# Optimization experiments

Measured on AMD Instinct MI355X. Metric: run time of the kernel, lower is better.

## Reference

```python
import jax, jax.numpy as jnp
import numpy as np

N_NODES = 100000
N_EDGES = 1600000
N_GRAPHS = 64
EMB_DIM = 64
DIMS = [6, 16, 32, 64, EMB_DIM]


def setup_inputs() -> dict:
    key = jax.random.key(0)
    ks = jax.random.split(key, 16)
    feat = jax.random.normal(ks[0], (N_NODES, DIMS[0]), dtype=jnp.float32)
    src = jax.random.randint(ks[1], (N_EDGES,), 0, N_NODES)
    dst = jax.random.randint(ks[2], (N_EDGES,), 0, N_NODES)
    graph_ids = jnp.sort(jax.random.randint(ks[3], (N_NODES,), 0, N_GRAPHS))
    inp = {"feat": feat, "src": src, "dst": dst, "graph_ids": graph_ids}
    # fc_neigh weights for each SAGEConv (gcn aggregator has no fc_self), Xavier-ish init
    for i in range(4):
        din, dout = DIMS[i], DIMS[i + 1]
        scale = 1.0 / np.sqrt(din)
        inp[f"W{i+1}"] = jax.random.uniform(ks[4 + 2 * i], (din, dout), jnp.float32, -scale, scale)
        inp[f"b{i+1}"] = jnp.zeros((dout,), jnp.float32)
    return inp


def _sage_gcn(feat, src, dst, deg, W, b):
    # DGL SAGEConv aggregator_type='gcn':
    # h_neigh = (sum_{u in N(v)} h_u + h_v) / (in_deg(v) + 1); out = h_neigh @ W + b
    neigh = jax.ops.segment_sum(feat[src], dst, num_segments=N_NODES)  # [N, din]
    h = (neigh + feat) / (deg[:, None] + 1.0)
    return h @ W + b


def reference(feat, src, dst, graph_ids, W1, b1, W2, b2, W3, b3, W4, b4):
    deg = jax.ops.segment_sum(jnp.ones((N_EDGES,), feat.dtype), dst, num_segments=N_NODES)
    h = feat
    for W, b in ((W1, b1), (W2, b2), (W3, b3), (W4, b4)):
        h = jax.nn.relu(_sage_gcn(h, src, dst, deg, W, b))
    # dgl.mean_nodes: per-graph mean over nodes
    sums = jax.ops.segment_sum(h, graph_ids, num_segments=N_GRAPHS)          # [G, emb]
    cnts = jax.ops.segment_sum(jnp.ones((N_NODES,), h.dtype), graph_ids, num_segments=N_GRAPHS)
    return sums / jnp.maximum(cnts, 1.0)[:, None]
```

## Files before the change

### kernel.cpp

```cpp
#include <hip/hip_runtime.h>
#include <hip/hip_bf16.h>
#include <hip/hip_fp16.h>

#define N_NODES 100000
#define N_EDGES 1600000
#define N_GRAPHS 64

#define NB_BKT 256
#define NPBKT 391
#define EPB 4096
#define NBLK_FEAT ((N_NODES + 255) / 256)
#define NBLK_BIN ((N_EDGES + EPB - 1) / EPB)
#define BKT_CAP 7168


__device__ __forceinline__ __half2 u2h(unsigned int u) {
    return __builtin_bit_cast(__half2, u);
}
__device__ __forceinline__ float2 u2f2(unsigned int u) {
    return __half22float2(u2h(u));
}
__device__ __forceinline__ unsigned int packh2(float a, float b) {
    return __builtin_bit_cast(unsigned int, __float22half2_rn(make_float2(a, b)));
}


__global__ __launch_bounds__(256) void prep(const float* __restrict__ feat,
                                            const int* __restrict__ dst,
                                            const int* __restrict__ src,
                                            uint4* __restrict__ feat16,
                                            int* __restrict__ gcur,
                                            uint2* __restrict__ rec, int n, int E) {
    __shared__ int cnt[NB_BKT];
    __shared__ int lbase[NB_BKT];
    __shared__ int gofs[NB_BKT];
    __shared__ uint2 stage[EPB];
    int t = threadIdx.x;

    if ((int)blockIdx.x < NBLK_FEAT) {
        __shared__ float sf[256 * 6];
        int b0 = blockIdx.x * 256;
        int c = min(256, n - b0) * 6;
        for (int i = t; i < c; i += 256) sf[i] = feat[(size_t)b0 * 6 + i];
        __syncthreads();
        int v = b0 + t;
        if (v < n) {
            const float* f = sf + t * 6;
            uint4 r;
            r.x = packh2(f[0], f[1]);
            r.y = packh2(f[2], f[3]);
            r.z = packh2(f[4], f[5]);
            r.w = 0u;
            feat16[v] = r;
        }
        return;
    }

    int e0 = (blockIdx.x - NBLK_FEAT) * EPB;
    cnt[t] = 0;
    __syncthreads();
    int myb[16], mypos[16];
    unsigned myd[16], mys[16];
#pragma unroll
    for (int k = 0; k < 16; ++k) {
        int e = e0 + k * 256 + t;
        if (e < E) {
            unsigned d = (unsigned)dst[e];
            int b = (int)(d / (unsigned)NPBKT);
            myd[k] = d;
            mys[k] = (unsigned)src[e];
            myb[k] = b;
            mypos[k] = atomicAdd(&cnt[b], 1);
        } else {
            myb[k] = -1;
        }
    }
    __syncthreads();
    int c = cnt[t];
    int res = (c > 0) ? atomicAdd(&gcur[t], c) : 0;
    lbase[t] = c;
    __syncthreads();
    for (int o = 1; o < 256; o <<= 1) {
        int a = (t >= o) ? lbase[t - o] : 0;
        __syncthreads();
        lbase[t] += a;
        __syncthreads();
    }
    lbase[t] -= c;
    gofs[t] = res;
    __syncthreads();
#pragma unroll
    for (int k = 0; k < 16; ++k)
        if (myb[k] >= 0) stage[lbase[myb[k]] + mypos[k]] = make_uint2(myd[k], mys[k]);
    __syncthreads();
    int total = min(EPB, E - e0);
    for (int i = t; i < total; i += 256) {
        int lo = 0, hi = NB_BKT - 1;
        while (lo < hi) {
            int m = (lo + hi + 1) >> 1;
            if (lbase[m] <= i) lo = m; else hi = m - 1;
        }
        rec[(size_t)lo * BKT_CAP + gofs[lo] + (i - lbase[lo])] = stage[i];
    }
}


__global__ __launch_bounds__(256) void fill_bucket(const uint2* __restrict__ rec,
                                                   const int* __restrict__ gcur,
                                                   int* __restrict__ rp,
                                                   int* __restrict__ col, int n) {
    __shared__ int sdeg[512];
    __shared__ int lcur[512];
    __shared__ int sg[256];
    __shared__ int lcol[8192];
    int p = blockIdx.x, t = threadIdx.x;
    int nbase = p * NPBKT;
    int nn = min(NPBKT, n - nbase);
    int g = gcur[t];
    sg[t] = g;
    __syncthreads();
    for (int o = 1; o < 256; o <<= 1) {
        int a = (t >= o) ? sg[t - o] : 0;
        __syncthreads();
        sg[t] += a;
        __syncthreads();
    }
    int ex = sg[t] - g;
    __syncthreads();
    sg[t] = ex;
    __syncthreads();
    int cbase = sg[p];
    int cnt = gcur[p];
    sdeg[t] = 0;
    sdeg[t + 256] = 0;
    __syncthreads();
    const uint2* r = rec + (size_t)p * BKT_CAP;
    for (int i = t; i < cnt; i += 256) atomicAdd(&sdeg[r[i].x - (unsigned)nbase], 1);
    __syncthreads();
    int c0 = sdeg[t], c1 = sdeg[t + 256];
    for (int o = 1; o < 512; o <<= 1) {
        int a = (t >= o) ? sdeg[t - o] : 0;
        int b = (t + 256 >= o) ? sdeg[t + 256 - o] : 0;
        __syncthreads();
        sdeg[t] += a;
        sdeg[t + 256] += b;
        __syncthreads();
    }
    int ex0 = sdeg[t] - c0, ex1 = sdeg[t + 256] - c1;
    lcur[t] = ex0;
    lcur[t + 256] = ex1;
    if (t < nn) rp[nbase + t] = cbase + ex0;
    if (t + 256 < nn) rp[nbase + t + 256] = cbase + ex1;
    if (p == NB_BKT - 1 && t == 0) rp[n] = cbase + cnt;
    __syncthreads();
    for (int i = t; i < cnt; i += 256) {
        uint2 e = r[i];
        int slot = atomicAdd(&lcur[e.x - (unsigned)nbase], 1);
        lcol[slot] = (int)e.y;
    }
    __syncthreads();
    for (int i = t; i < cnt; i += 256) col[cbase + i] = lcol[i];
}


template <int DIN, int DOUT, int TB>
__global__ __launch_bounds__(TB) void sage_f16(const uint4* __restrict__ hin,
                                               const int* __restrict__ rp,
                                               const int* __restrict__ col,
                                               const float* __restrict__ W,
                                               const float* __restrict__ bias,
                                               unsigned int* __restrict__ hout,
                                               int real_din, int n) {
    constexpr int WPN = DIN / 8;
    constexpr int NPB = TB / WPN;
    constexpr int OPT = DOUT / WPN;
    __shared__ float sW[DIN * DOUT];
    __shared__ float sB[DOUT];
    __shared__ float sH[NPB][DIN + 1];

    int tid = threadIdx.x;
    for (int i = tid; i < DIN * DOUT; i += TB) sW[i] = (i < real_din * DOUT) ? W[i] : 0.f;
    if (tid < DOUT) sB[tid] = bias[tid];

    int sub = tid / WPN;
    int t = tid % WPN;
    int v = blockIdx.x * NPB + sub;

    if (v < n) {
        int r0 = rp[v], r1 = rp[v + 1];
        const __half2 z = __float2half2_rn(0.f);
        __half2 acc[4][4];
#pragma unroll
        for (int s = 0; s < 4; ++s)
#pragma unroll
            for (int q = 0; q < 4; ++q) acc[s][q] = z;
        int j = r0;
        for (; j + 8 <= r1; j += 8) {
            uint4 w[8];
#pragma unroll
            for (int k = 0; k < 8; ++k) w[k] = hin[col[j + k] * WPN + t];
#pragma unroll
            for (int k = 0; k < 8; ++k) {
                __half2* a = acc[k & 3];
                a[0] = __hadd2(a[0], u2h(w[k].x));
                a[1] = __hadd2(a[1], u2h(w[k].y));
                a[2] = __hadd2(a[2], u2h(w[k].z));
                a[3] = __hadd2(a[3], u2h(w[k].w));
            }
        }
        for (; j + 4 <= r1; j += 4) {
            uint4 w[4];
#pragma unroll
            for (int k = 0; k < 4; ++k) w[k] = hin[col[j + k] * WPN + t];
#pragma unroll
            for (int k = 0; k < 4; ++k) {
                __half2* a = acc[k];
                a[0] = __hadd2(a[0], u2h(w[k].x));
                a[1] = __hadd2(a[1], u2h(w[k].y));
                a[2] = __hadd2(a[2], u2h(w[k].z));
                a[3] = __hadd2(a[3], u2h(w[k].w));
            }
        }
        for (; j < r1; ++j) {
            uint4 w = hin[col[j] * WPN + t];
            acc[0][0] = __hadd2(acc[0][0], u2h(w.x));
            acc[0][1] = __hadd2(acc[0][1], u2h(w.y));
            acc[0][2] = __hadd2(acc[0][2], u2h(w.z));
            acc[0][3] = __hadd2(acc[0][3], u2h(w.w));
        }
#pragma unroll
        for (int q = 0; q < 4; ++q)
            acc[0][q] = __hadd2(__hadd2(acc[0][q], acc[1][q]),
                                __hadd2(acc[2][q], acc[3][q]));
        uint4 ws = hin[v * WPN + t];
        unsigned swd[4] = {ws.x, ws.y, ws.z, ws.w};
        float inv = 1.0f / (float)(r1 - r0 + 1);
#pragma unroll
        for (int q = 0; q < 4; ++q) {
            float2 f = __half22float2(acc[0][q]);
            float2 s = u2f2(swd[q]);
            sH[sub][t * 8 + 2 * q + 0] = (f.x + s.x) * inv;
            sH[sub][t * 8 + 2 * q + 1] = (f.y + s.y) * inv;
        }
    }
    __syncthreads();
    if (v < n) {
        int o0 = t * OPT;
        float accO[OPT];
#pragma unroll
        for (int i = 0; i < OPT; ++i) accO[i] = sB[o0 + i];
#pragma unroll 4
        for (int k = 0; k < DIN; ++k) {
            float hk = sH[sub][k];
#pragma unroll
            for (int i = 0; i < OPT; ++i) accO[i] += hk * sW[k * DOUT + o0 + i];
        }
        unsigned wds[OPT / 2];
#pragma unroll
        for (int i = 0; i < OPT; i += 2)
            wds[i / 2] = packh2(fmaxf(accO[i], 0.f), fmaxf(accO[i + 1], 0.f));
        unsigned* op = hout + v * (DOUT / 2) + o0 / 2;
        if constexpr (OPT / 2 == 4) {
            *reinterpret_cast<uint4*>(op) = make_uint4(wds[0], wds[1], wds[2], wds[3]);
        } else if constexpr (OPT / 2 == 8) {
            reinterpret_cast<uint4*>(op)[0] = make_uint4(wds[0], wds[1], wds[2], wds[3]);
            reinterpret_cast<uint4*>(op)[1] = make_uint4(wds[4], wds[5], wds[6], wds[7]);
        } else {
            *reinterpret_cast<uint2*>(op) = make_uint2(wds[0], wds[1]);
        }
    }
}


__device__ __forceinline__ int lower_bound_i(const int* __restrict__ a, int n, int key) {
    int lo = 0, hi = n;
    while (lo < hi) {
        int m = (lo + hi) >> 1;
        if (a[m] < key) lo = m + 1; else hi = m;
    }
    return lo;
}

__global__ __launch_bounds__(256) void pool_f16(const unsigned int* __restrict__ h32,
                                                const int* __restrict__ gids,
                                                float* __restrict__ out, int n) {
    int bx = blockIdx.x;
    int g = bx >> 3, s = bx & 7;
    int start = lower_bound_i(gids, n, g);
    int end = lower_bound_i(gids, n, g + 1);
    int len = end - start;
    float inv = 1.0f / (float)(len > 0 ? len : 1);
    int chunk = (len + 7) / 8;
    int s0 = start + s * chunk;
    int s1 = min(s0 + chunk, end);
    int t = threadIdx.x;
    int d = t & 31, j = t >> 5;
    float a0 = 0.f, a1 = 0.f;
    for (int i = s0 + j; i < s1; i += 8) {
        float2 f = u2f2(h32[(size_t)i * 32 + d]);
        a0 += f.x;
        a1 += f.y;
    }
    __shared__ float red[8][32][2];
    red[j][d][0] = a0;
    red[j][d][1] = a1;
    __syncthreads();
    if (t < 64) {
        int dd = t & 31, e = t >> 5;
        float tot = 0.f;
#pragma unroll
        for (int k = 0; k < 8; ++k) tot += red[k][dd][e];
        atomicAdd(&out[g * 64 + 2 * dd + e], tot * inv);
    }
}


extern "C" void kernel_launch(void* const* d_in, const int* in_sizes, int n_in,
                              void* d_out, int out_size, void* d_ws, size_t ws_size,
                              hipStream_t stream) {
    const int N = N_NODES, E = N_EDGES;
    const float* feat = (const float*)d_in[0];
    const int* src = (const int*)d_in[1];
    const int* dst = (const int*)d_in[2];
    const int* gids = (const int*)d_in[3];
    const float* W1 = (const float*)d_in[4];
    const float* b1 = (const float*)d_in[5];
    const float* W2 = (const float*)d_in[6];
    const float* b2 = (const float*)d_in[7];
    const float* W3 = (const float*)d_in[8];
    const float* b3 = (const float*)d_in[9];
    const float* W4 = (const float*)d_in[10];
    const float* b4 = (const float*)d_in[11];
    float* out = (float*)d_out;

    int* rp = (int*)d_ws;
    int* gcur = rp + (N + 1);
    int* col = gcur + 256;
    size_t off = (size_t)((char*)(col + E) - (char*)d_ws);
    off = (off + 255) & ~(size_t)255;
    unsigned int* h1 = (unsigned int*)((char*)d_ws + off);
    unsigned int* h2 = h1 + (size_t)N * 8;
    unsigned int* h3 = h2 + (size_t)N * 16;
    unsigned int* h4 = h3 + (size_t)N * 32;
    uint4* feat16 = (uint4*)(h4 + (size_t)N * 32);
    uint2* rec = (uint2*)h3;

    hipMemsetAsync(out, 0, (size_t)N_GRAPHS * 64 * sizeof(float), stream);
    hipMemsetAsync(gcur, 0, 256 * sizeof(int), stream);

    prep<<<NBLK_FEAT + NBLK_BIN, 256, 0, stream>>>(feat, dst, src, feat16, gcur, rec, N, E);
    fill_bucket<<<NB_BKT, 256, 0, stream>>>(rec, gcur, rp, col, N);

    sage_f16<8, 16, 256><<<(N + 255) / 256, 256, 0, stream>>>(
        feat16, rp, col, W1, b1, h1, 6, N);
    sage_f16<16, 32, 512><<<(N + 255) / 256, 512, 0, stream>>>(
        (const uint4*)h1, rp, col, W2, b2, h2, 16, N);
    sage_f16<32, 64, 512><<<(N + 127) / 128, 512, 0, stream>>>(
        (const uint4*)h2, rp, col, W3, b3, h3, 32, N);
    sage_f16<64, 64, 512><<<(N + 63) / 64, 512, 0, stream>>>(
        (const uint4*)h3, rp, col, W4, b4, h4, 64, N);

    pool_f16<<<N_GRAPHS * 8, 256, 0, stream>>>(h4, gids, out, N);
}
```

Baseline: 185.7 us.

## Sort nodes by in-degree within buckets to balance warp work in SAGE layers

fill_bucket now counting-sorts the nodes of each bucket by in-degree into a permutation array. Every sage_f16 layer processes nodes in that order, so each wavefront handles nodes of similar degree and the gather loop diverges less. The cost is an extra histogram, scan and scatter in fill_bucket, one more indirect load per node, and scattered output writes that lose coalescing.

Result: slower. 191.1 us (+2.9%).

```diff
diff --git a/kernel.cpp b/kernel.cpp
--- a/kernel.cpp
+++ b/kernel.cpp
@@ -108,10 +108,12 @@
 __global__ __launch_bounds__(256) void fill_bucket(const uint2* __restrict__ rec,
                                                    const int* __restrict__ gcur,
                                                    int* __restrict__ rp,
-                                                   int* __restrict__ col, int n) {
+                                                   int* __restrict__ col,
+                                                   int* __restrict__ perm, int n) {
     __shared__ int sdeg[512];
     __shared__ int lcur[512];
     __shared__ int sg[256];
+    __shared__ int hist[256];
     __shared__ int lcol[8192];
     int p = blockIdx.x, t = threadIdx.x;
     int nbase = p * NPBKT;
@@ -160,6 +162,28 @@
     }
     __syncthreads();
     for (int i = t; i < cnt; i += 256) col[cbase + i] = lcol[i];
+
+    hist[t] = 0;
+    __syncthreads();
+    int b0 = -1, rk0 = 0, b1 = -1, rk1 = 0;
+    if (t < nn) { b0 = min(c0, 255); rk0 = atomicAdd(&hist[b0], 1); }
+    if (t + 256 < nn) { b1 = min(c1, 255); rk1 = atomicAdd(&hist[b1], 1); }
+    __syncthreads();
+    int hv = hist[t];
+    sg[t] = hv;
+    __syncthreads();
+    for (int o = 1; o < 256; o <<= 1) {
+        int a = (t >= o) ? sg[t - o] : 0;
+        __syncthreads();
+        sg[t] += a;
+        __syncthreads();
+    }
+    int hb = sg[t] - hv;
+    __syncthreads();
+    sg[t] = hb;
+    __syncthreads();
+    if (t < nn) perm[nbase + sg[b0] + rk0] = nbase + t;
+    if (t + 256 < nn) perm[nbase + sg[b1] + rk1] = nbase + t + 256;
 }
 
 
@@ -167,6 +191,7 @@
 __global__ __launch_bounds__(TB) void sage_f16(const uint4* __restrict__ hin,
                                                const int* __restrict__ rp,
                                                const int* __restrict__ col,
+                                               const int* __restrict__ perm,
                                                const float* __restrict__ W,
                                                const float* __restrict__ bias,
                                                unsigned int* __restrict__ hout,
@@ -184,9 +209,10 @@
 
     int sub = tid / WPN;
     int t = tid % WPN;
-    int v = blockIdx.x * NPB + sub;
-
-    if (v < n) {
+    int pos = blockIdx.x * NPB + sub;
+    int v = (pos < n) ? perm[pos] : -1;
+
+    if (v >= 0) {
         int r0 = rp[v], r1 = rp[v + 1];
         const __half2 z = __float2half2_rn(0.f);
         __half2 acc[4][4];
@@ -244,7 +270,7 @@
         }
     }
     __syncthreads();
-    if (v < n) {
+    if (v >= 0) {
         int o0 = t * OPT;
         float accO[OPT];
 #pragma unroll
@@ -335,7 +361,8 @@
 
     int* rp = (int*)d_ws;
     int* gcur = rp + (N + 1);
-    int* col = gcur + 256;
+    int* perm = gcur + 256;
+    int* col = perm + N;
     size_t off = (size_t)((char*)(col + E) - (char*)d_ws);
     off = (off + 255) & ~(size_t)255;
     unsigned int* h1 = (unsigned int*)((char*)d_ws + off);
@@ -349,16 +376,16 @@
     hipMemsetAsync(gcur, 0, 256 * sizeof(int), stream);
 
     prep<<<NBLK_FEAT + NBLK_BIN, 256, 0, stream>>>(feat, dst, src, feat16, gcur, rec, N, E);
-    fill_bucket<<<NB_BKT, 256, 0, stream>>>(rec, gcur, rp, col, N);
+    fill_bucket<<<NB_BKT, 256, 0, stream>>>(rec, gcur, rp, col, perm, N);
 
     sage_f16<8, 16, 256><<<(N + 255) / 256, 256, 0, stream>>>(
-        feat16, rp, col, W1, b1, h1, 6, N);
+        feat16, rp, col, perm, W1, b1, h1, 6, N);
     sage_f16<16, 32, 512><<<(N + 255) / 256, 512, 0, stream>>>(
-        (const uint4*)h1, rp, col, W2, b2, h2, 16, N);
+        (const uint4*)h1, rp, col, perm, W2, b2, h2, 16, N);
     sage_f16<32, 64, 512><<<(N + 127) / 128, 512, 0, stream>>>(
-        (const uint4*)h2, rp, col, W3, b3, h3, 32, N);
+        (const uint4*)h2, rp, col, perm, W3, b3, h3, 32, N);
     sage_f16<64, 64, 512><<<(N + 63) / 64, 512, 0, stream>>>(
-        (const uint4*)h3, rp, col, W4, b4, h4, 64, N);
+        (const uint4*)h3, rp, col, perm, W4, b4, h4, 64, N);
 
     pool_f16<<<N_GRAPHS * 8, 256, 0, stream>>>(h4, gids, out, N);
 }
```
